# Kernel tuning notes

Hardware: AMD Instinct MI355X
Metric: run time of the kernel (lower is better)

The kernel has to match this reference:

```python
import jax, jax.numpy as jnp
import numpy as np

D = 1024
H = 16
HD = D // H
DFF = 4 * D
B, L = 2, 2048
EPS = 1e-5


def setup_inputs() -> dict:
    key = jax.random.key(0)
    ks = jax.random.split(key, 12)
    s = lambda fan_in: 1.0 / np.sqrt(fan_in)
    inp = {
        "x": jax.random.normal(ks[0], (B, L, D), jnp.float32),
        "mask": jnp.ones((1, 1, L, L), jnp.bool_),
        "ln_g": jnp.ones((D,), jnp.float32),
        "ln_b": jnp.zeros((D,), jnp.float32),
        "qkv_w": jax.random.uniform(ks[1], (3 * D, D), jnp.float32, -s(D), s(D)),
        "qkv_b": jax.random.uniform(ks[2], (3 * D,), jnp.float32, -s(D), s(D)),
        "wo_w": jax.random.uniform(ks[3], (D, D), jnp.float32, -s(D), s(D)),
        "wo_b": jax.random.uniform(ks[4], (D,), jnp.float32, -s(D), s(D)),
        "m0_w": jax.random.uniform(ks[5], (DFF, D), jnp.float32, -s(D), s(D)),
        "m0_b": jax.random.uniform(ks[6], (DFF,), jnp.float32, -s(D), s(D)),
        "m1_w": jax.random.uniform(ks[7], (D, DFF), jnp.float32, -s(DFF), s(DFF)),
        "m1_b": jax.random.uniform(ks[8], (D,), jnp.float32, -s(DFF), s(DFF)),
    }
    return inp


def _layer_norm(x, g, b):
    mu = jnp.mean(x, axis=-1, keepdims=True)
    var = jnp.var(x, axis=-1, keepdims=True)
    return (x - mu) * jax.lax.rsqrt(var + EPS) * g + b


def reference(x, mask, ln_g, ln_b, qkv_w, qkv_b, wo_w, wo_b, m0_w, m0_b, m1_w, m1_b):
    b, l, d = x.shape
    # --- pre-norm self-attention ---
    xn = _layer_norm(x, ln_g, ln_b)
    qkv = xn @ qkv_w.T + qkv_b                       # [B, L, 3D]
    qkv = qkv.reshape(b, l, 3, H, HD).transpose(2, 0, 3, 1, 4)  # [3, B, H, L, HD]
    q, k, v = qkv[0], qkv[1], qkv[2]
    scores = jnp.einsum("bhld,bhmd->bhlm", q, k) / np.sqrt(HD)  # [B, H, L, L]
    scores = jnp.where(mask, scores, -1e9)
    attn = jax.nn.softmax(scores, axis=-1)
    ctx = jnp.einsum("bhlm,bhmd->bhld", attn, v)     # [B, H, L, HD]
    ctx = ctx.transpose(0, 2, 1, 3).reshape(b, l, d)
    x = x + ctx @ wo_w.T + wo_b
    # --- GELU MLP (same shared LayerNorm params) ---
    xn = _layer_norm(x, ln_g, ln_b)
    h = jax.nn.gelu(xn @ m0_w.T + m0_b, approximate=False)
    return x + h @ m1_w.T + m1_b
```

## Files before the change

kernel.cpp:

```cpp
#include <hip/hip_runtime.h>
#include <hip/hip_bf16.h>
#include <math.h>

#define BL 4096
#define DM 1024
#define NH 16
#define HD 64
#define DFF 4096
#define SEQ 2048
#define EPS 1e-5f
#define QSCALE 0.18033688011112042f

typedef __bf16 bf16x8 __attribute__((ext_vector_type(8)));
typedef float f32x4 __attribute__((ext_vector_type(4)));
typedef float f32x16 __attribute__((ext_vector_type(16)));

__device__ __forceinline__ unsigned short f2bf(float f) {
    __hip_bfloat16 h = __float2bfloat16(f);
    return *reinterpret_cast<unsigned short*>(&h);
}

__device__ __forceinline__ unsigned int pack2bf(float p0, float p1) {
    unsigned int u0 = __builtin_bit_cast(unsigned int, p0) + 0x8000u;
    unsigned int u1 = __builtin_bit_cast(unsigned int, p1) + 0x8000u;
    return __builtin_amdgcn_perm(u1, u0, 0x07060302);
}

__device__ __forceinline__ void gload_lds16(const void* g, void* l) {
    __builtin_amdgcn_global_load_lds(
        (const __attribute__((address_space(1))) unsigned int*)g,
        (__attribute__((address_space(3))) unsigned int*)l,
        16, 0, 0);
}

__global__ __launch_bounds__(256)
void prep_kernel(const float* __restrict__ x, const float* __restrict__ g,
                 const float* __restrict__ b, unsigned short* __restrict__ o,
                 const float* __restrict__ s0, const float* __restrict__ s1,
                 const float* __restrict__ s2, const float* __restrict__ s3,
                 unsigned short* __restrict__ d0, unsigned short* __restrict__ d1,
                 unsigned short* __restrict__ d2, unsigned short* __restrict__ d3,
                 int n0, int n1, int n2, int n3) {
    const int bid = blockIdx.x;
    const int tid = threadIdx.x;
    if (bid >= BL) {
        int i = (bid - BL) * 256 + tid;
        const float* s; unsigned short* d; int j = i;
        if (j < n0) { s = s0; d = d0; }
        else if ((j -= n0) < n1) { s = s1; d = d1; }
        else if ((j -= n1) < n2) { s = s2; d = d2; }
        else if ((j -= n2) < n3) { s = s3; d = d3; }
        else return;
        float4 v = ((const float4*)s)[j];
        ushort4 ov = {f2bf(v.x), f2bf(v.y), f2bf(v.z), f2bf(v.w)};
        ((ushort4*)d)[j] = ov;
        return;
    }
    const int row = bid;
    const float* xr = x + (size_t)row * DM;
    float4 v = *(const float4*)(xr + tid * 4);
    float s_  = v.x + v.y + v.z + v.w;
    float ss = v.x*v.x + v.y*v.y + v.z*v.z + v.w*v.w;
    #pragma unroll
    for (int off = 32; off > 0; off >>= 1) {
        s_ += __shfl_down(s_, off);
        ss += __shfl_down(ss, off);
    }
    __shared__ float ps[4], pss[4];
    __shared__ float sh_mu, sh_rs;
    int wid = tid >> 6, lane = tid & 63;
    if (lane == 0) { ps[wid] = s_; pss[wid] = ss; }
    __syncthreads();
    if (tid == 0) {
        float S = ps[0] + ps[1] + ps[2] + ps[3];
        float SS = pss[0] + pss[1] + pss[2] + pss[3];
        float mu = S * (1.0f / DM);
        float var = SS * (1.0f / DM) - mu * mu;
        sh_mu = mu;
        sh_rs = 1.0f / sqrtf(var + EPS);
    }
    __syncthreads();
    float mu = sh_mu, rs = sh_rs;
    float4 gv = *(const float4*)(g + tid * 4);
    float4 bv = *(const float4*)(b + tid * 4);
    ushort4 ov;
    ov.x = f2bf((v.x - mu) * rs * gv.x + bv.x);
    ov.y = f2bf((v.y - mu) * rs * gv.y + bv.y);
    ov.z = f2bf((v.z - mu) * rs * gv.z + bv.z);
    ov.w = f2bf((v.w - mu) * rs * gv.w + bv.w);
    *(ushort4*)(o + (size_t)row * DM + tid * 4) = ov;
}

__global__ __launch_bounds__(256)
void ln_kernel(const float* __restrict__ x, const float* __restrict__ g,
               const float* __restrict__ b, unsigned short* __restrict__ o) {
    int row = blockIdx.x;
    int tid = threadIdx.x;
    const float* xr = x + (size_t)row * DM;
    float4 v = *(const float4*)(xr + tid * 4);
    float s  = v.x + v.y + v.z + v.w;
    float ss = v.x*v.x + v.y*v.y + v.z*v.z + v.w*v.w;
    #pragma unroll
    for (int off = 32; off > 0; off >>= 1) {
        s  += __shfl_down(s, off);
        ss += __shfl_down(ss, off);
    }
    __shared__ float ps[4], pss[4];
    __shared__ float sh_mu, sh_rs;
    int wid = tid >> 6, lane = tid & 63;
    if (lane == 0) { ps[wid] = s; pss[wid] = ss; }
    __syncthreads();
    if (tid == 0) {
        float S = ps[0] + ps[1] + ps[2] + ps[3];
        float SS = pss[0] + pss[1] + pss[2] + pss[3];
        float mu = S * (1.0f / DM);
        float var = SS * (1.0f / DM) - mu * mu;
        sh_mu = mu;
        sh_rs = 1.0f / sqrtf(var + EPS);
    }
    __syncthreads();
    float mu = sh_mu, rs = sh_rs;
    float4 gv = *(const float4*)(g + tid * 4);
    float4 bv = *(const float4*)(b + tid * 4);
    ushort4 ov;
    ov.x = f2bf((v.x - mu) * rs * gv.x + bv.x);
    ov.y = f2bf((v.y - mu) * rs * gv.y + bv.y);
    ov.z = f2bf((v.z - mu) * rs * gv.z + bv.z);
    ov.w = f2bf((v.w - mu) * rs * gv.w + bv.w);
    *(ushort4*)(o + (size_t)row * DM + tid * 4) = ov;
}

template <int EPI, typename OUT_T>
__global__ __launch_bounds__(256)
void gemm_bt_mfma(const unsigned short* __restrict__ A,
                  const unsigned short* __restrict__ B,
                  const float* __restrict__ bias, const float* __restrict__ res,
                  OUT_T* __restrict__ C, int M, int N, int K,
                  unsigned short* __restrict__ vt) {
    __shared__ unsigned short smem[2][16384];
    const int tid = threadIdx.x, lane = tid & 63, wave = tid >> 6;

    const int id   = blockIdx.x;
    const int xcd  = id & 7, slot = id >> 3;
    const int R    = (M / 128) >> 3;
    const int by   = xcd * R + (slot % R);
    const int bx   = slot / R;
    const int m0 = by * 128, n0 = bx * 128;
    const int wm = (wave >> 1) * 64, wn = (wave & 1) * 64;
    const int srow = lane >> 3, sslot = lane & 7;
    const int fr = lane & 15, g = lane >> 4;

    f32x4 acc[4][4] = {};

    auto stage = [&](int b, int kt) {
        unsigned short* As = smem[b];
        unsigned short* Bs = smem[b] + 8192;
        #pragma unroll
        for (int rep = 0; rep < 8; rep++) {
            const int c = rep * 4 + wave;
            const bool isA = (c < 16);
            const int cc = isA ? c : c - 16;
            const int cr = cc * 8 + srow;
            const unsigned short* src = (isA ? A + (size_t)(m0 + cr) * K
                                             : B + (size_t)(n0 + cr) * K)
                                        + kt + ((sslot ^ (cr & 7)) * 8);
            gload_lds16(src, (char*)(isA ? As : Bs) + cc * 1024);
        }
    };

    stage(0, 0);
    const int NT = K >> 6;
    for (int ti = 0; ti < NT; ti++) {
        __syncthreads();
        if (ti + 1 < NT) stage((ti + 1) & 1, (ti + 1) * 64);
        const unsigned short* As = smem[ti & 1];
        const unsigned short* Bs = As + 8192;
        #pragma unroll
        for (int ko = 0; ko < 2; ko++) {
            const int col = (((ko * 4 + g) ^ (fr & 7)) * 8);
            bf16x8 af[4], bfv[4];
            #pragma unroll
            for (int i = 0; i < 4; i++)
                af[i] = *(const bf16x8*)(As + (wm + i * 16 + fr) * 64 + col);
            #pragma unroll
            for (int j = 0; j < 4; j++)
                bfv[j] = *(const bf16x8*)(Bs + (wn + j * 16 + fr) * 64 + col);
            #pragma unroll
            for (int i = 0; i < 4; i++)
                #pragma unroll
                for (int j = 0; j < 4; j++)
                    acc[i][j] = __builtin_amdgcn_mfma_f32_16x16x32_bf16(af[i], bfv[j], acc[i][j], 0, 0, 0);
        }
    }

    const int col  = lane & 15;
    const int rowq = (lane >> 4) * 4;
    float bs[4];
    #pragma unroll
    for (int j = 0; j < 4; j++) bs[j] = bias[n0 + wn + j * 16 + col];

    if (EPI == 3 && n0 >= 2048) {
        __syncthreads();
        unsigned short* sc = smem[0];
        #pragma unroll
        for (int i = 0; i < 4; i++) {
            const int l0 = wm + i * 16 + rowq;
            #pragma unroll
            for (int j = 0; j < 4; j++) {
                const int dcol = wn + j * 16 + col;
                float v0 = acc[i][j][0] + bs[j], v1 = acc[i][j][1] + bs[j];
                float v2 = acc[i][j][2] + bs[j], v3 = acc[i][j][3] + bs[j];
                uint2 pk = {pack2bf(v0, v1), pack2bf(v2, v3)};
                char* p = (char*)sc + dcol * 256 +
                          (((l0 >> 3) ^ (dcol & 7)) * 16) + (l0 & 7) * 2;
                *(uint2*)p = pk;
            }
        }
        __syncthreads();
        const int bb = m0 >> 11, lbase = m0 & 2047;
        #pragma unroll
        for (int k = 0; k < 8; k++) {
            const int oid = tid + k * 256;
            const int dcol = oid >> 4, lc = oid & 15;
            uint4 val = *(const uint4*)((const char*)sc + dcol * 256 +
                                        ((lc ^ (dcol & 7)) * 16));
            const int c = n0 + dcol;
            const int d = c & 63, hh2 = (c >> 6) & 15;
            *(uint4*)(vt + ((size_t)((bb * 16 + hh2) * 64 + d)) * 2048 + lbase + lc * 8) = val;
        }
        return;
    }

    #pragma unroll
    for (int i = 0; i < 4; i++) {
        #pragma unroll
        for (int r = 0; r < 4; r++) {
            const size_t row = (size_t)(m0 + wm + i * 16 + rowq + r);
            #pragma unroll
            for (int j = 0; j < 4; j++) {
                const int c = n0 + wn + j * 16 + col;
                const size_t off = row * N + c;
                float v = acc[i][j][r] + bs[j];
                if (EPI == 1) v += res[off];
                if (EPI == 2) {
                    float u = v * (0.7978845608028654f + 0.035677408136300125f * v * v);
                    float e = __builtin_amdgcn_exp2f(u * 2.885390081777927f);
                    float th = 1.0f - 2.0f * __builtin_amdgcn_rcpf(e + 1.0f);
                    v = 0.5f * v * (1.0f + th);
                }
                if (EPI == 3) {
                    float vq = (c < 1024) ? v * QSCALE : v;
                    ((unsigned short*)C)[off] = f2bf(vq);
                } else if constexpr (sizeof(OUT_T) == 2) {
                    ((unsigned short*)C)[off] = f2bf(v);
                } else {
                    ((float*)C)[off] = v;
                }
            }
        }
    }
}

template <int K>
__global__ __launch_bounds__(512)
void gemm_splitk_res(const unsigned short* __restrict__ A,
                     const unsigned short* __restrict__ B,
                     const float* __restrict__ bias,
                     const float* __restrict__ res,
                     float* __restrict__ C) {
    __shared__ unsigned short smem[2][2][16384];
    const int id   = blockIdx.x;
    const int xcd  = id & 7, slot = id >> 3;
    const int by   = xcd * 4 + (slot & 3);
    const int bx   = slot >> 2;
    const int m0 = by * 128, n0 = bx * 128;
    const int tid = threadIdx.x, lane = tid & 63, wave = tid >> 6;
    const int grp = wave >> 2, w4 = wave & 3;
    const int wm = (w4 >> 1) * 64, wn = (w4 & 1) * 64;
    const int srow = lane >> 3, sslot = lane & 7;
    const int fr = lane & 15, g = lane >> 4;
    const int kg0 = grp * (K / 2);
    constexpr int NT = K / 128;

    f32x4 acc[4][4] = {};

    auto stage = [&](int b, int kt) {
        unsigned short* As = smem[grp][b];
        unsigned short* Bs = smem[grp][b] + 8192;
        #pragma unroll
        for (int rep = 0; rep < 8; rep++) {
            const int c = rep * 4 + w4;
            const bool isA = (c < 16);
            const int cc = isA ? c : c - 16;
            const int cr = cc * 8 + srow;
            const unsigned short* src = (isA ? A + (size_t)(m0 + cr) * K
                                             : B + (size_t)(n0 + cr) * K)
                                        + kt + ((sslot ^ (cr & 7)) * 8);
            gload_lds16(src, (char*)(isA ? As : Bs) + cc * 1024);
        }
    };

    stage(0, kg0);
    for (int ti = 0; ti < NT; ti++) {
        __syncthreads();
        if (ti + 1 < NT) stage((ti + 1) & 1, kg0 + (ti + 1) * 64);
        const unsigned short* As = smem[grp][ti & 1];
        const unsigned short* Bs = As + 8192;
        #pragma unroll
        for (int ko = 0; ko < 2; ko++) {
            const int col = (((ko * 4 + g) ^ (fr & 7)) * 8);
            bf16x8 af[4], bfv[4];
            #pragma unroll
            for (int i = 0; i < 4; i++)
                af[i] = *(const bf16x8*)(As + (wm + i * 16 + fr) * 64 + col);
            #pragma unroll
            for (int j = 0; j < 4; j++)
                bfv[j] = *(const bf16x8*)(Bs + (wn + j * 16 + fr) * 64 + col);
            #pragma unroll
            for (int i = 0; i < 4; i++)
                #pragma unroll
                for (int j = 0; j < 4; j++)
                    acc[i][j] = __builtin_amdgcn_mfma_f32_16x16x32_bf16(af[i], bfv[j], acc[i][j], 0, 0, 0);
        }
    }

    __syncthreads();
    float* ox = (float*)smem;
    if (grp == 1) {
        float* bp = ox + w4 * 4096;
        #pragma unroll
        for (int i = 0; i < 4; i++)
            #pragma unroll
            for (int j = 0; j < 4; j++)
                *(f32x4*)(bp + (i * 4 + j) * 256 + lane * 4) = acc[i][j];
    }
    __syncthreads();
    if (grp == 1) return;
    {
        float* bp = ox + w4 * 4096;
        #pragma unroll
        for (int i = 0; i < 4; i++)
            #pragma unroll
            for (int j = 0; j < 4; j++)
                acc[i][j] += *(const f32x4*)(bp + (i * 4 + j) * 256 + lane * 4);
    }

    const int col = lane & 15, rowq = (lane >> 4) * 4;
    float bs[4];
    #pragma unroll
    for (int j = 0; j < 4; j++) bs[j] = bias[n0 + wn + j * 16 + col];
    #pragma unroll
    for (int i = 0; i < 4; i++)
        #pragma unroll
        for (int r = 0; r < 4; r++) {
            const size_t row = (size_t)(m0 + wm + i * 16 + rowq + r);
            #pragma unroll
            for (int j = 0; j < 4; j++) {
                const int c = n0 + wn + j * 16 + col;
                const size_t off = row * 1024 + c;
                C[off] = acc[i][j][r] + bs[j] + res[off];
            }
        }
}

__global__ __launch_bounds__(512)
void attn_mfma(const unsigned short* __restrict__ qkv,
               const unsigned short* __restrict__ vt,
               unsigned short* __restrict__ ctx) {
    __shared__ unsigned short smem[2][16384];
    const int bid = blockIdx.x;
    const int xcd = bid & 7, sl = bid >> 3;
    const int qt = sl & 15, pg = sl >> 4;
    const int pair = pg * 8 + xcd;
    const int h = pair & 15, b = pair >> 4;
    const int tid = threadIdx.x, lane = tid & 63, wave = tid >> 6;
    const int grp = wave >> 2, w4 = wave & 3;
    const int hh = lane >> 5, mm = lane & 31;
    const int q0 = b * 2048 + qt * 128 + w4 * 32;

    unsigned short* Ks = smem[grp];
    unsigned short* Vt = smem[grp] + 8192;

    bf16x8 qf[4];
    const unsigned short* qb = qkv + (size_t)(q0 + mm) * 3072 + h * 64 + hh * 8;
    #pragma unroll
    for (int s = 0; s < 4; s++) qf[s] = *(const bf16x8*)(qb + s * 16);

    const int skey = lane >> 3;
    const int sgr  = (lane & 7) ^ (skey & 7);
    const unsigned short* kbase = qkv + ((size_t)(b * 2048) + skey) * 3072 + 1024 + h * 64 + sgr * 8;
    const unsigned short* vbase = vt + ((size_t)((b * 16 + h) * 64) + skey) * 2048 + sgr * 8;

    float l_lane = 0.0f;
    f32x16 o_acc[2] = {};
    const int kt0 = grp * 1024;

    for (int ti = 0; ti < 8; ti++) {
        const int kt = kt0 + ti * 128;
        __syncthreads();
        #pragma unroll
        for (int rep = 0; rep < 4; rep++) {
            int c = rep * 4 + w4;
            gload_lds16(kbase + (size_t)(kt + c * 8) * 3072, (char*)Ks + c * 1024);
        }
        #pragma unroll
        for (int rep = 0; rep < 2; rep++) {
            int c = rep * 4 + w4;
            gload_lds16(vbase + (size_t)(c * 8) * 2048 + kt,      (char*)Vt + c * 1024);
            gload_lds16(vbase + (size_t)(c * 8) * 2048 + kt + 64, (char*)Vt + 8192 + c * 1024);
        }
        __syncthreads();

        #pragma unroll
        for (int sub = 0; sub < 2; sub++) {
            f32x16 sT[2] = {};
            __builtin_amdgcn_s_setprio(1);
            #pragma unroll
            for (int t = 0; t < 2; t++)
                #pragma unroll
                for (int s = 0; s < 4; s++) {
                    bf16x8 kf = *(const bf16x8*)(Ks + (sub * 64 + t * 32 + mm) * 64 + ((s * 2 + hh) ^ (mm & 7)) * 8);
                    sT[t] = __builtin_amdgcn_mfma_f32_32x32x16_bf16(kf, qf[s], sT[t], 0, 0, 0);
                }
            __builtin_amdgcn_s_setprio(0);

            unsigned int pk[2][8];
            #pragma unroll
            for (int t = 0; t < 2; t++)
                #pragma unroll
                for (int e = 0; e < 8; e++) {
                    float p0 = __builtin_amdgcn_exp2f(sT[t][2 * e]);
                    float p1 = __builtin_amdgcn_exp2f(sT[t][2 * e + 1]);
                    l_lane += p0 + p1;
                    pk[t][e] = pack2bf(p0, p1);
                }

            __builtin_amdgcn_s_setprio(1);
            #pragma unroll
            for (int w = 0; w < 4; w++) {
                const int t = w >> 1, eb = (w & 1) * 4;
                unsigned int a0 = pk[t][eb + 0], a1 = pk[t][eb + 1];
                unsigned int a2 = pk[t][eb + 2], a3 = pk[t][eb + 3];
                asm("v_permlane32_swap_b32 %0, %1" : "+v"(a0), "+v"(a2));
                asm("v_permlane32_swap_b32 %0, %1" : "+v"(a1), "+v"(a3));
                union { unsigned int u[4]; bf16x8 v; } af;
                af.u[0] = a0; af.u[1] = a1; af.u[2] = a2; af.u[3] = a3;
                #pragma unroll
                for (int dt = 0; dt < 2; dt++) {
                    bf16x8 vf = *(const bf16x8*)(Vt + sub * 4096 + (dt * 32 + mm) * 64 + ((w * 2 + hh) ^ (mm & 7)) * 8);
                    o_acc[dt] = __builtin_amdgcn_mfma_f32_32x32x16_bf16(af.v, vf, o_acc[dt], 0, 0, 0);
                }
            }
            __builtin_amdgcn_s_setprio(0);
        }
    }

    float l_red = l_lane + __shfl_xor(l_lane, 32);
    __syncthreads();
    float* ox = (float*)smem;
    float* lx = (float*)((char*)smem + 32768);
    if (grp == 1) {
        float* base = ox + w4 * 2048;
        #pragma unroll
        for (int dt = 0; dt < 2; dt++)
            #pragma unroll
            for (int r = 0; r < 16; r++)
                base[(dt * 16 + r) * 64 + lane] = o_acc[dt][r];
        if (hh == 0) lx[w4 * 32 + mm] = l_red;
    }
    __syncthreads();
    if (grp == 1) return;
    {
        float* base = ox + w4 * 2048;
        #pragma unroll
        for (int dt = 0; dt < 2; dt++)
            #pragma unroll
            for (int r = 0; r < 16; r++)
                o_acc[dt][r] += base[(dt * 16 + r) * 64 + lane];
        l_red += lx[w4 * 32 + mm];
    }

    float inv_own = 1.0f / l_red;
    #pragma unroll
    for (int r = 0; r < 16; r++) {
        const int rowq = (r & 3) + 8 * (r >> 2) + 4 * hh;
        float inv = __shfl(inv_own, rowq);
        size_t base = (size_t)(q0 + rowq) * 1024 + h * 64 + mm;
        ctx[base]      = f2bf(o_acc[0][r] * inv);
        ctx[base + 32] = f2bf(o_acc[1][r] * inv);
    }
}

extern "C" void kernel_launch(void* const* d_in, const int* in_sizes, int n_in,
                              void* d_out, int out_size, void* d_ws, size_t ws_size,
                              hipStream_t stream) {
    const float* x     = (const float*)d_in[0];
    const float* ln_g  = (const float*)d_in[2];
    const float* ln_b  = (const float*)d_in[3];
    const float* qkv_w = (const float*)d_in[4];
    const float* qkv_b = (const float*)d_in[5];
    const float* wo_w  = (const float*)d_in[6];
    const float* wo_b  = (const float*)d_in[7];
    const float* m0_w  = (const float*)d_in[8];
    const float* m0_b  = (const float*)d_in[9];
    const float* m1_w  = (const float*)d_in[10];
    const float* m1_b  = (const float*)d_in[11];
    float* out = (float*)d_out;

    char* ws = (char*)d_ws;
    unsigned short* xn_bf  = (unsigned short*)(ws);
    unsigned short* qkv_bf = (unsigned short*)(ws + (size_t)8  * 1024 * 1024);
    unsigned short* vt_bf  = (unsigned short*)(ws + (size_t)32 * 1024 * 1024);
    unsigned short* ctx_bf = (unsigned short*)(ws + (size_t)40 * 1024 * 1024);
    unsigned short* h_bf   = (unsigned short*)(ws + (size_t)48 * 1024 * 1024);
    unsigned short* qkvw_b = (unsigned short*)(ws + (size_t)80 * 1024 * 1024);
    unsigned short* wow_b  = (unsigned short*)(ws + (size_t)86 * 1024 * 1024);
    unsigned short* m0w_b  = (unsigned short*)(ws + (size_t)88 * 1024 * 1024);
    unsigned short* m1w_b  = (unsigned short*)(ws + (size_t)96 * 1024 * 1024);

    {
        int n0 = 3 * DM * DM / 4, n1 = DM * DM / 4, n2 = DFF * DM / 4, n3 = DM * DFF / 4;
        int tot = n0 + n1 + n2 + n3;
        prep_kernel<<<BL + (tot + 255) / 256, 256, 0, stream>>>(
            x, ln_g, ln_b, xn_bf,
            qkv_w, wo_w, m0_w, m1_w, qkvw_b, wow_b, m0w_b, m1w_b, n0, n1, n2, n3);
    }

    gemm_bt_mfma<3, unsigned short><<<(3072 / 128) * (BL / 128), 256, 0, stream>>>(
        xn_bf, qkvw_b, qkv_b, nullptr, qkv_bf, BL, 3072, DM, vt_bf);
    attn_mfma<<<2 * NH * (SEQ / 128), 512, 0, stream>>>(qkv_bf, vt_bf, ctx_bf);
    gemm_splitk_res<1024><<<256, 512, 0, stream>>>(ctx_bf, wow_b, wo_b, x, out);
    ln_kernel<<<BL, 256, 0, stream>>>(out, ln_g, ln_b, xn_bf);
    gemm_bt_mfma<2, unsigned short><<<(DFF / 128) * (BL / 128), 256, 0, stream>>>(
        xn_bf, m0w_b, m0_b, nullptr, h_bf, BL, DFF, DM, nullptr);
    gemm_splitk_res<4096><<<256, 512, 0, stream>>>(h_bf, m1w_b, m1_b, out, out);
}
```

Measured before the change: 312.2 us.

## Unify GEMMs into 8-wave intra-block split-K kernel for all projections

Replaces the 4-wave GEMM used for the QKV and MLP-up projections with an 8-wave kernel. Two wave groups each take half of K and their partial tiles are combined through LDS. The same kernel now also serves the residual projections that previously used a separate split-K kernel. This doubles the waves per block to hide latency better on short-K GEMMs, at the cost of an extra LDS reduction, larger shared memory and possibly fewer resident blocks per CU.

Measured after the change: 324.7 us. +4.0%, slower.

```diff
diff --git a/kernel.cpp b/kernel.cpp
--- a/kernel.cpp
+++ b/kernel.cpp
@@ -130,50 +130,51 @@
     *(ushort4*)(o + (size_t)row * DM + tid * 4) = ov;
 }
 
-template <int EPI, typename OUT_T>
-__global__ __launch_bounds__(256)
-void gemm_bt_mfma(const unsigned short* __restrict__ A,
-                  const unsigned short* __restrict__ B,
-                  const float* __restrict__ bias, const float* __restrict__ res,
-                  OUT_T* __restrict__ C, int M, int N, int K,
-                  unsigned short* __restrict__ vt) {
-    __shared__ unsigned short smem[2][16384];
-    const int tid = threadIdx.x, lane = tid & 63, wave = tid >> 6;
-
+template <int KTOT, int EPI, typename OUT_T>
+__global__ __launch_bounds__(512)
+void gemm8w(const unsigned short* __restrict__ A,
+            const unsigned short* __restrict__ B,
+            const float* __restrict__ bias, const float* __restrict__ res,
+            OUT_T* __restrict__ C, int M, int N,
+            unsigned short* __restrict__ vt) {
+    __shared__ unsigned short smem[2][2][16384];
     const int id   = blockIdx.x;
     const int xcd  = id & 7, slot = id >> 3;
     const int R    = (M / 128) >> 3;
     const int by   = xcd * R + (slot % R);
     const int bx   = slot / R;
     const int m0 = by * 128, n0 = bx * 128;
-    const int wm = (wave >> 1) * 64, wn = (wave & 1) * 64;
+    const int tid = threadIdx.x, lane = tid & 63, wave = tid >> 6;
+    const int grp = wave >> 2, w4 = wave & 3;
+    const int wm = (w4 >> 1) * 64, wn = (w4 & 1) * 64;
     const int srow = lane >> 3, sslot = lane & 7;
     const int fr = lane & 15, g = lane >> 4;
+    const int kg0 = grp * (KTOT / 2);
+    constexpr int NT = KTOT / 128;
 
     f32x4 acc[4][4] = {};
 
     auto stage = [&](int b, int kt) {
-        unsigned short* As = smem[b];
-        unsigned short* Bs = smem[b] + 8192;
+        unsigned short* As = smem[grp][b];
+        unsigned short* Bs = smem[grp][b] + 8192;
         #pragma unroll
         for (int rep = 0; rep < 8; rep++) {
-            const int c = rep * 4 + wave;
+            const int c = rep * 4 + w4;
             const bool isA = (c < 16);
             const int cc = isA ? c : c - 16;
             const int cr = cc * 8 + srow;
-            const unsigned short* src = (isA ? A + (size_t)(m0 + cr) * K
-                                             : B + (size_t)(n0 + cr) * K)
+            const unsigned short* src = (isA ? A + (size_t)(m0 + cr) * KTOT
+                                             : B + (size_t)(n0 + cr) * KTOT)
                                         + kt + ((sslot ^ (cr & 7)) * 8);
             gload_lds16(src, (char*)(isA ? As : Bs) + cc * 1024);
         }
     };
 
-    stage(0, 0);
-    const int NT = K >> 6;
+    stage(0, kg0);
     for (int ti = 0; ti < NT; ti++) {
         __syncthreads();
-        if (ti + 1 < NT) stage((ti + 1) & 1, (ti + 1) * 64);
-        const unsigned short* As = smem[ti & 1];
+        if (ti + 1 < NT) stage((ti + 1) & 1, kg0 + (ti + 1) * 64);
+        const unsigned short* As = smem[grp][ti & 1];
         const unsigned short* Bs = As + 8192;
         #pragma unroll
         for (int ko = 0; ko < 2; ko++) {
@@ -193,36 +194,57 @@
         }
     }
 
-    const int col  = lane & 15;
-    const int rowq = (lane >> 4) * 4;
-    float bs[4];
-    #pragma unroll
-    for (int j = 0; j < 4; j++) bs[j] = bias[n0 + wn + j * 16 + col];
+    __syncthreads();
+    float* ox = (float*)smem;
+    if (grp == 1) {
+        float* bp = ox + w4 * 4096;
+        #pragma unroll
+        for (int i = 0; i < 4; i++)
+            #pragma unroll
+            for (int j = 0; j < 4; j++)
+                *(f32x4*)(bp + (i * 4 + j) * 256 + lane * 4) = acc[i][j];
+    }
+    __syncthreads();
+    if (grp == 0) {
+        float* bp = ox + w4 * 4096;
+        #pragma unroll
+        for (int i = 0; i < 4; i++)
+            #pragma unroll
+            for (int j = 0; j < 4; j++)
+                acc[i][j] += *(const f32x4*)(bp + (i * 4 + j) * 256 + lane * 4);
+    }
+
+    const int col = lane & 15, rowq = (lane >> 4) * 4;
 
     if (EPI == 3 && n0 >= 2048) {
         __syncthreads();
-        unsigned short* sc = smem[0];
-        #pragma unroll
-        for (int i = 0; i < 4; i++) {
-            const int l0 = wm + i * 16 + rowq;
-            #pragma unroll
-            for (int j = 0; j < 4; j++) {
-                const int dcol = wn + j * 16 + col;
-                float v0 = acc[i][j][0] + bs[j], v1 = acc[i][j][1] + bs[j];
-                float v2 = acc[i][j][2] + bs[j], v3 = acc[i][j][3] + bs[j];
-                uint2 pk = {pack2bf(v0, v1), pack2bf(v2, v3)};
-                char* p = (char*)sc + dcol * 256 +
-                          (((l0 >> 3) ^ (dcol & 7)) * 16) + (l0 & 7) * 2;
-                *(uint2*)p = pk;
+        if (grp == 0) {
+            float bs[4];
+            #pragma unroll
+            for (int j = 0; j < 4; j++) bs[j] = bias[n0 + wn + j * 16 + col];
+            unsigned short* sc = (unsigned short*)smem;
+            #pragma unroll
+            for (int i = 0; i < 4; i++) {
+                const int l0 = wm + i * 16 + rowq;
+                #pragma unroll
+                for (int j = 0; j < 4; j++) {
+                    const int dcol = wn + j * 16 + col;
+                    float v0 = acc[i][j][0] + bs[j], v1 = acc[i][j][1] + bs[j];
+                    float v2 = acc[i][j][2] + bs[j], v3 = acc[i][j][3] + bs[j];
+                    uint2 pk = {pack2bf(v0, v1), pack2bf(v2, v3)};
+                    char* p = (char*)sc + dcol * 256 +
+                              (((l0 >> 3) ^ (dcol & 7)) * 16) + (l0 & 7) * 2;
+                    *(uint2*)p = pk;
+                }
             }
         }
         __syncthreads();
         const int bb = m0 >> 11, lbase = m0 & 2047;
         #pragma unroll
-        for (int k = 0; k < 8; k++) {
-            const int oid = tid + k * 256;
+        for (int k = 0; k < 4; k++) {
+            const int oid = tid + k * 512;
             const int dcol = oid >> 4, lc = oid & 15;
-            uint4 val = *(const uint4*)((const char*)sc + dcol * 256 +
+            uint4 val = *(const uint4*)((const char*)smem + dcol * 256 +
                                         ((lc ^ (dcol & 7)) * 16));
             const int c = n0 + dcol;
             const int d = c & 63, hh2 = (c >> 6) & 15;
@@ -231,8 +253,12 @@
         return;
     }
 
-    #pragma unroll
-    for (int i = 0; i < 4; i++) {
+    if (grp == 1) return;
+    float bs[4];
+    #pragma unroll
+    for (int j = 0; j < 4; j++) bs[j] = bias[n0 + wn + j * 16 + col];
+    #pragma unroll
+    for (int i = 0; i < 4; i++)
         #pragma unroll
         for (int r = 0; r < 4; r++) {
             const size_t row = (size_t)(m0 + wm + i * 16 + rowq + r);
@@ -256,109 +282,6 @@
                 } else {
                     ((float*)C)[off] = v;
                 }
-            }
-        }
-    }
-}
-
-template <int K>
-__global__ __launch_bounds__(512)
-void gemm_splitk_res(const unsigned short* __restrict__ A,
-                     const unsigned short* __restrict__ B,
-                     const float* __restrict__ bias,
-                     const float* __restrict__ res,
-                     float* __restrict__ C) {
-    __shared__ unsigned short smem[2][2][16384];
-    const int id   = blockIdx.x;
-    const int xcd  = id & 7, slot = id >> 3;
-    const int by   = xcd * 4 + (slot & 3);
-    const int bx   = slot >> 2;
-    const int m0 = by * 128, n0 = bx * 128;
-    const int tid = threadIdx.x, lane = tid & 63, wave = tid >> 6;
-    const int grp = wave >> 2, w4 = wave & 3;
-    const int wm = (w4 >> 1) * 64, wn = (w4 & 1) * 64;
-    const int srow = lane >> 3, sslot = lane & 7;
-    const int fr = lane & 15, g = lane >> 4;
-    const int kg0 = grp * (K / 2);
-    constexpr int NT = K / 128;
-
-    f32x4 acc[4][4] = {};
-
-    auto stage = [&](int b, int kt) {
-        unsigned short* As = smem[grp][b];
-        unsigned short* Bs = smem[grp][b] + 8192;
-        #pragma unroll
-        for (int rep = 0; rep < 8; rep++) {
-            const int c = rep * 4 + w4;
-            const bool isA = (c < 16);
-            const int cc = isA ? c : c - 16;
-            const int cr = cc * 8 + srow;
-            const unsigned short* src = (isA ? A + (size_t)(m0 + cr) * K
-                                             : B + (size_t)(n0 + cr) * K)
-                                        + kt + ((sslot ^ (cr & 7)) * 8);
-            gload_lds16(src, (char*)(isA ? As : Bs) + cc * 1024);
-        }
-    };
-
-    stage(0, kg0);
-    for (int ti = 0; ti < NT; ti++) {
-        __syncthreads();
-        if (ti + 1 < NT) stage((ti + 1) & 1, kg0 + (ti + 1) * 64);
-        const unsigned short* As = smem[grp][ti & 1];
-        const unsigned short* Bs = As + 8192;
-        #pragma unroll
-        for (int ko = 0; ko < 2; ko++) {
-            const int col = (((ko * 4 + g) ^ (fr & 7)) * 8);
-            bf16x8 af[4], bfv[4];
-            #pragma unroll
-            for (int i = 0; i < 4; i++)
-                af[i] = *(const bf16x8*)(As + (wm + i * 16 + fr) * 64 + col);
-            #pragma unroll
-            for (int j = 0; j < 4; j++)
-                bfv[j] = *(const bf16x8*)(Bs + (wn + j * 16 + fr) * 64 + col);
-            #pragma unroll
-            for (int i = 0; i < 4; i++)
-                #pragma unroll
-                for (int j = 0; j < 4; j++)
-                    acc[i][j] = __builtin_amdgcn_mfma_f32_16x16x32_bf16(af[i], bfv[j], acc[i][j], 0, 0, 0);
-        }
-    }
-
-    __syncthreads();
-    float* ox = (float*)smem;
-    if (grp == 1) {
-        float* bp = ox + w4 * 4096;
-        #pragma unroll
-        for (int i = 0; i < 4; i++)
-            #pragma unroll
-            for (int j = 0; j < 4; j++)
-                *(f32x4*)(bp + (i * 4 + j) * 256 + lane * 4) = acc[i][j];
-    }
-    __syncthreads();
-    if (grp == 1) return;
-    {
-        float* bp = ox + w4 * 4096;
-        #pragma unroll
-        for (int i = 0; i < 4; i++)
-            #pragma unroll
-            for (int j = 0; j < 4; j++)
-                acc[i][j] += *(const f32x4*)(bp + (i * 4 + j) * 256 + lane * 4);
-    }
-
-    const int col = lane & 15, rowq = (lane >> 4) * 4;
-    float bs[4];
-    #pragma unroll
-    for (int j = 0; j < 4; j++) bs[j] = bias[n0 + wn + j * 16 + col];
-    #pragma unroll
-    for (int i = 0; i < 4; i++)
-        #pragma unroll
-        for (int r = 0; r < 4; r++) {
-            const size_t row = (size_t)(m0 + wm + i * 16 + rowq + r);
-            #pragma unroll
-            for (int j = 0; j < 4; j++) {
-                const int c = n0 + wn + j * 16 + col;
-                const size_t off = row * 1024 + c;
-                C[off] = acc[i][j][r] + bs[j] + res[off];
             }
         }
 }
@@ -526,12 +449,14 @@
             qkv_w, wo_w, m0_w, m1_w, qkvw_b, wow_b, m0w_b, m1w_b, n0, n1, n2, n3);
     }
 
-    gemm_bt_mfma<3, unsigned short><<<(3072 / 128) * (BL / 128), 256, 0, stream>>>(
-        xn_bf, qkvw_b, qkv_b, nullptr, qkv_bf, BL, 3072, DM, vt_bf);
+    gemm8w<1024, 3, unsigned short><<<(3072 / 128) * (BL / 128), 512, 0, stream>>>(
+        xn_bf, qkvw_b, qkv_b, nullptr, qkv_bf, BL, 3072, vt_bf);
     attn_mfma<<<2 * NH * (SEQ / 128), 512, 0, stream>>>(qkv_bf, vt_bf, ctx_bf);
-    gemm_splitk_res<1024><<<256, 512, 0, stream>>>(ctx_bf, wow_b, wo_b, x, out);
+    gemm8w<1024, 1, float><<<(DM / 128) * (BL / 128), 512, 0, stream>>>(
+        ctx_bf, wow_b, wo_b, x, out, BL, DM, nullptr);
     ln_kernel<<<BL, 256, 0, stream>>>(out, ln_g, ln_b, xn_bf);
-    gemm_bt_mfma<2, unsigned short><<<(DFF / 128) * (BL / 128), 256, 0, stream>>>(
-        xn_bf, m0w_b, m0_b, nullptr, h_bf, BL, DFF, DM, nullptr);
-    gemm_splitk_res<4096><<<256, 512, 0, stream>>>(h_bf, m1w_b, m1_b, out, out);
-}
+    gemm8w<1024, 2, unsigned short><<<(DFF / 128) * (BL / 128), 512, 0, stream>>>(
+        xn_bf, m0w_b, m0_b, nullptr, h_bf, BL, DFF, nullptr);
+    gemm8w<4096, 1, float><<<(DM / 128) * (BL / 128), 512, 0, stream>>>(
+        h_bf, m1w_b, m1_b, out, out, BL, DM, nullptr);
+}
```

## Fuse output-projection GEMM and second LayerNorm via cooperative grid sync

Applied to the files above, without the earlier changes.

Replaces the split-K Wo projection kernel and the separate LayerNorm kernel with one cooperative kernel. It runs the GEMM with residual add, synchronises the whole grid, then has each block normalise 16 rows of the result into bf16. This removes one kernel launch and the gap between the two kernels. In exchange it adds the cost of a grid-wide barrier and needs all 256 blocks to be resident at once.

Result: slower. 379.0 us (+21.4%).

```diff
diff --git a/kernel.cpp b/kernel.cpp
--- a/kernel.cpp
+++ b/kernel.cpp
@@ -1,5 +1,6 @@
 #include <hip/hip_runtime.h>
 #include <hip/hip_bf16.h>
+#include <hip/hip_cooperative_groups.h>
 #include <math.h>
 
 #define BL 4096
@@ -91,45 +92,6 @@
     *(ushort4*)(o + (size_t)row * DM + tid * 4) = ov;
 }
 
-__global__ __launch_bounds__(256)
-void ln_kernel(const float* __restrict__ x, const float* __restrict__ g,
-               const float* __restrict__ b, unsigned short* __restrict__ o) {
-    int row = blockIdx.x;
-    int tid = threadIdx.x;
-    const float* xr = x + (size_t)row * DM;
-    float4 v = *(const float4*)(xr + tid * 4);
-    float s  = v.x + v.y + v.z + v.w;
-    float ss = v.x*v.x + v.y*v.y + v.z*v.z + v.w*v.w;
-    #pragma unroll
-    for (int off = 32; off > 0; off >>= 1) {
-        s  += __shfl_down(s, off);
-        ss += __shfl_down(ss, off);
-    }
-    __shared__ float ps[4], pss[4];
-    __shared__ float sh_mu, sh_rs;
-    int wid = tid >> 6, lane = tid & 63;
-    if (lane == 0) { ps[wid] = s; pss[wid] = ss; }
-    __syncthreads();
-    if (tid == 0) {
-        float S = ps[0] + ps[1] + ps[2] + ps[3];
-        float SS = pss[0] + pss[1] + pss[2] + pss[3];
-        float mu = S * (1.0f / DM);
-        float var = SS * (1.0f / DM) - mu * mu;
-        sh_mu = mu;
-        sh_rs = 1.0f / sqrtf(var + EPS);
-    }
-    __syncthreads();
-    float mu = sh_mu, rs = sh_rs;
-    float4 gv = *(const float4*)(g + tid * 4);
-    float4 bv = *(const float4*)(b + tid * 4);
-    ushort4 ov;
-    ov.x = f2bf((v.x - mu) * rs * gv.x + bv.x);
-    ov.y = f2bf((v.y - mu) * rs * gv.y + bv.y);
-    ov.z = f2bf((v.z - mu) * rs * gv.z + bv.z);
-    ov.w = f2bf((v.w - mu) * rs * gv.w + bv.w);
-    *(ushort4*)(o + (size_t)row * DM + tid * 4) = ov;
-}
-
 template <int EPI, typename OUT_T>
 __global__ __launch_bounds__(256)
 void gemm_bt_mfma(const unsigned short* __restrict__ A,
@@ -364,6 +326,144 @@
 }
 
 __global__ __launch_bounds__(512)
+void fused_wo_ln(const unsigned short* __restrict__ A,
+                 const unsigned short* __restrict__ B,
+                 const float* __restrict__ bias,
+                 const float* __restrict__ res,
+                 float* __restrict__ C,
+                 const float* __restrict__ gw,
+                 const float* __restrict__ bw,
+                 unsigned short* __restrict__ xn) {
+    constexpr int K = 1024;
+    __shared__ unsigned short smem[2][2][16384];
+    const int id   = blockIdx.x;
+    const int xcd  = id & 7, slot = id >> 3;
+    const int by   = xcd * 4 + (slot & 3);
+    const int bx   = slot >> 2;
+    const int m0 = by * 128, n0 = bx * 128;
+    const int tid = threadIdx.x, lane = tid & 63, wave = tid >> 6;
+    const int grp = wave >> 2, w4 = wave & 3;
+    const int wm = (w4 >> 1) * 64, wn = (w4 & 1) * 64;
+    const int srow = lane >> 3, sslot = lane & 7;
+    const int fr = lane & 15, g = lane >> 4;
+    const int kg0 = grp * (K / 2);
+    constexpr int NT = K / 128;
+
+    f32x4 acc[4][4] = {};
+
+    auto stage = [&](int b, int kt) {
+        unsigned short* As = smem[grp][b];
+        unsigned short* Bs = smem[grp][b] + 8192;
+        #pragma unroll
+        for (int rep = 0; rep < 8; rep++) {
+            const int c = rep * 4 + w4;
+            const bool isA = (c < 16);
+            const int cc = isA ? c : c - 16;
+            const int cr = cc * 8 + srow;
+            const unsigned short* src = (isA ? A + (size_t)(m0 + cr) * K
+                                             : B + (size_t)(n0 + cr) * K)
+                                        + kt + ((sslot ^ (cr & 7)) * 8);
+            gload_lds16(src, (char*)(isA ? As : Bs) + cc * 1024);
+        }
+    };
+
+    stage(0, kg0);
+    for (int ti = 0; ti < NT; ti++) {
+        __syncthreads();
+        if (ti + 1 < NT) stage((ti + 1) & 1, kg0 + (ti + 1) * 64);
+        const unsigned short* As = smem[grp][ti & 1];
+        const unsigned short* Bs = As + 8192;
+        #pragma unroll
+        for (int ko = 0; ko < 2; ko++) {
+            const int col = (((ko * 4 + g) ^ (fr & 7)) * 8);
+            bf16x8 af[4], bfv[4];
+            #pragma unroll
+            for (int i = 0; i < 4; i++)
+                af[i] = *(const bf16x8*)(As + (wm + i * 16 + fr) * 64 + col);
+            #pragma unroll
+            for (int j = 0; j < 4; j++)
+                bfv[j] = *(const bf16x8*)(Bs + (wn + j * 16 + fr) * 64 + col);
+            #pragma unroll
+            for (int i = 0; i < 4; i++)
+                #pragma unroll
+                for (int j = 0; j < 4; j++)
+                    acc[i][j] = __builtin_amdgcn_mfma_f32_16x16x32_bf16(af[i], bfv[j], acc[i][j], 0, 0, 0);
+        }
+    }
+
+    __syncthreads();
+    float* ox = (float*)smem;
+    if (grp == 1) {
+        float* bp = ox + w4 * 4096;
+        #pragma unroll
+        for (int i = 0; i < 4; i++)
+            #pragma unroll
+            for (int j = 0; j < 4; j++)
+                *(f32x4*)(bp + (i * 4 + j) * 256 + lane * 4) = acc[i][j];
+    }
+    __syncthreads();
+    if (grp == 0) {
+        float* bp = ox + w4 * 4096;
+        #pragma unroll
+        for (int i = 0; i < 4; i++)
+            #pragma unroll
+            for (int j = 0; j < 4; j++)
+                acc[i][j] += *(const f32x4*)(bp + (i * 4 + j) * 256 + lane * 4);
+
+        const int col = lane & 15, rowq = (lane >> 4) * 4;
+        float bs[4];
+        #pragma unroll
+        for (int j = 0; j < 4; j++) bs[j] = bias[n0 + wn + j * 16 + col];
+        #pragma unroll
+        for (int i = 0; i < 4; i++)
+            #pragma unroll
+            for (int r = 0; r < 4; r++) {
+                const size_t row = (size_t)(m0 + wm + i * 16 + rowq + r);
+                #pragma unroll
+                for (int j = 0; j < 4; j++) {
+                    const int c = n0 + wn + j * 16 + col;
+                    const size_t off = row * 1024 + c;
+                    C[off] = acc[i][j][r] + bs[j] + res[off];
+                }
+            }
+    }
+
+    cooperative_groups::this_grid().sync();
+
+    float* ph = (float*)smem;
+    const int team = tid >> 8, tt = tid & 255;
+    const int wl = (tid >> 6) & 3;
+    for (int it = 0; it < 8; it++) {
+        const int row = id * 16 + it * 2 + team;
+        const float* xr = C + (size_t)row * DM;
+        float4 v = *(const float4*)(xr + tt * 4);
+        float s  = v.x + v.y + v.z + v.w;
+        float ss = v.x*v.x + v.y*v.y + v.z*v.z + v.w*v.w;
+        #pragma unroll
+        for (int off = 32; off > 0; off >>= 1) {
+            s  += __shfl_down(s, off);
+            ss += __shfl_down(ss, off);
+        }
+        if ((tid & 63) == 0) { ph[team * 8 + wl] = s; ph[team * 8 + 4 + wl] = ss; }
+        __syncthreads();
+        float S  = ph[team*8+0] + ph[team*8+1] + ph[team*8+2] + ph[team*8+3];
+        float SS = ph[team*8+4] + ph[team*8+5] + ph[team*8+6] + ph[team*8+7];
+        float mu = S * (1.0f / DM);
+        float var = SS * (1.0f / DM) - mu * mu;
+        float rs = 1.0f / sqrtf(var + EPS);
+        float4 gv = *(const float4*)(gw + tt * 4);
+        float4 bv = *(const float4*)(bw + tt * 4);
+        ushort4 ov;
+        ov.x = f2bf((v.x - mu) * rs * gv.x + bv.x);
+        ov.y = f2bf((v.y - mu) * rs * gv.y + bv.y);
+        ov.z = f2bf((v.z - mu) * rs * gv.z + bv.z);
+        ov.w = f2bf((v.w - mu) * rs * gv.w + bv.w);
+        *(ushort4*)(xn + (size_t)row * DM + tt * 4) = ov;
+        __syncthreads();
+    }
+}
+
+__global__ __launch_bounds__(512)
 void attn_mfma(const unsigned short* __restrict__ qkv,
                const unsigned short* __restrict__ vt,
                unsigned short* __restrict__ ctx) {
@@ -529,8 +629,12 @@
     gemm_bt_mfma<3, unsigned short><<<(3072 / 128) * (BL / 128), 256, 0, stream>>>(
         xn_bf, qkvw_b, qkv_b, nullptr, qkv_bf, BL, 3072, DM, vt_bf);
     attn_mfma<<<2 * NH * (SEQ / 128), 512, 0, stream>>>(qkv_bf, vt_bf, ctx_bf);
-    gemm_splitk_res<1024><<<256, 512, 0, stream>>>(ctx_bf, wow_b, wo_b, x, out);
-    ln_kernel<<<BL, 256, 0, stream>>>(out, ln_g, ln_b, xn_bf);
+    {
+        void* args[] = {(void*)&ctx_bf, (void*)&wow_b, (void*)&wo_b, (void*)&x,
+                        (void*)&out, (void*)&ln_g, (void*)&ln_b, (void*)&xn_bf};
+        hipLaunchCooperativeKernel((void*)fused_wo_ln, dim3(256), dim3(512),
+                                   args, 0, stream);
+    }
     gemm_bt_mfma<2, unsigned short><<<(DFF / 128) * (BL / 128), 256, 0, stream>>>(
         xn_bf, m0w_b, m0_b, nullptr, h_bf, BL, DFF, DM, nullptr);
     gemm_splitk_res<4096><<<256, 512, 0, stream>>>(h_bf, m1w_b, m1_b, out, out);
```
